# Kernel tuning notes

Measured on AMD Instinct MI355X. Metric: run time of the kernel, lower is better.

The kernel has to match this reference:

```python
import jax, jax.numpy as jnp
import numpy as np

B, T, IN, H, OUT, L = 1024, 128, 32, 256, 32, 3  # batch, times, input_dim, hidden_dim, output_dim, num_layers
STEP = 0.05  # odeint rk4 step_size; times grid is aligned to it


def lipswish(x):
    return 0.909 * x * jax.nn.sigmoid(x)


def setup_inputs() -> dict:
    key = jax.random.key(0)
    ks = jax.random.split(key, 4)
    coeffs = jax.random.normal(ks[0], (B, T, IN), dtype=jnp.float32)
    times = jnp.arange(T, dtype=jnp.float32) * STEP
    # learned parameters
    W_init = jax.random.normal(ks[1], (IN, H), dtype=jnp.float32) * (1.0 / np.sqrt(IN))
    b_init = jnp.zeros((H,), dtype=jnp.float32)
    # vector field f: L lipswish hidden layers + final linear, all H->H
    Wf = jax.random.normal(ks[2], (L + 1, H, H), dtype=jnp.float32) * (1.0 / np.sqrt(H))
    bf = jnp.zeros((L + 1, H), dtype=jnp.float32)
    Wd = jax.random.normal(ks[3], (H, OUT), dtype=jnp.float32) * (1.0 / np.sqrt(H))
    bd = jnp.zeros((OUT,), dtype=jnp.float32)
    return dict(coeffs=coeffs, times=times, W_init=W_init, b_init=b_init,
                Wf=Wf, bf=bf, Wd=Wd, bd=bd)


def reference(coeffs, times, W_init, b_init, Wf, bf, Wd, bd):
    # vector field func.f(t, y): autonomous MLP (inject_noise=False, so g unused)
    def f(y):
        h = y
        for i in range(L):
            h = lipswish(h @ Wf[i] + bf[i])
        return h @ Wf[L] + bf[L]

    # y0 = initial(X.evaluate(times))[:, 0, :] -> only the first time point seeds the state
    y0 = coeffs[:, 0, :] @ W_init + b_init  # [B, H]

    dts = times[1:] - times[:-1]  # each interval = one RK4 step (grid aligned to step_size)

    def step(y, dt):
        k1 = f(y)
        k2 = f(y + 0.5 * dt * k1)
        k3 = f(y + 0.5 * dt * k2)
        k4 = f(y + dt * k3)
        y_next = y + (dt / 6.0) * (k1 + 2.0 * k2 + 2.0 * k3 + k4)
        return y_next, y_next

    _, ys = jax.lax.scan(step, y0, dts)  # [T-1, B, H]
    z = jnp.concatenate([y0[None], ys], axis=0)  # [T, B, H]
    z = jnp.transpose(z, (1, 0, 2))  # [B, T, H]
    return z @ Wd + bd  # [B, T, OUT]
```

## Files before the change

### kernel.cpp

```cpp
#include <hip/hip_runtime.h>


#define T_ 128
#define IN_ 32
#define H_ 256

typedef _Float16 half8 __attribute__((ext_vector_type(8)));
typedef _Float16 half4 __attribute__((ext_vector_type(4)));
typedef float f32x4 __attribute__((ext_vector_type(4)));

__device__ __forceinline__ f32x4 mfma16(half8 a, half8 b, f32x4 c) {
    return __builtin_amdgcn_mfma_f32_16x16x32_f16(a, b, c, 0, 0, 0);
}

__device__ __forceinline__ half4 cvt4(f32x4 v) {
    half4 h;
    h[0] = (_Float16)v[0]; h[1] = (_Float16)v[1];
    h[2] = (_Float16)v[2]; h[3] = (_Float16)v[3];
    return h;
}

__device__ __forceinline__ f32x4 lips4(f32x4 v) {
    f32x4 r;
#pragma unroll
    for (int e = 0; e < 4; ++e) {
        float x = v[e];
        r[e] = 0.909f * x * __builtin_amdgcn_rcpf(1.f + __expf(-x));
    }
    return r;
}

#define RDH(KS, BUF) (*(const half8*)(ht + (BUF) + (((KS) & 1) ? (po + ((KS)-1)*64) : (pe + (KS)*64))))
#define RDA(C, KS)   (*(const half8*)(w0b + (C)*8192 + (KS)*1024))

#define KSTEP(LYI, KS, BREG) \
    acc0 = mfma16(wreg[LYI][0][KS], BREG, acc0); \
    acc1 = mfma16(wreg[LYI][1][KS], BREG, acc1);

#define LAYER_REG(LYI, BUF) do {                    \
    half8 b0 = RDH(0, BUF), b1 = RDH(1, BUF);       \
    KSTEP(LYI, 0, b0) b0 = RDH(2, BUF);             \
    KSTEP(LYI, 1, b1) b1 = RDH(3, BUF);             \
    KSTEP(LYI, 2, b0) b0 = RDH(4, BUF);             \
    KSTEP(LYI, 3, b1) b1 = RDH(5, BUF);             \
    KSTEP(LYI, 4, b0) b0 = RDH(6, BUF);             \
    KSTEP(LYI, 5, b1) b1 = RDH(7, BUF);             \
    KSTEP(LYI, 6, b0)                               \
    KSTEP(LYI, 7, b1)                               \
} while (0)

#define KSTEP0(KS, BREG) {                              \
    half8 x;                                            \
    x = RDA(0, KS); acc0 = mfma16(x, BREG, acc0);       \
    x = RDA(1, KS); acc1 = mfma16(x, BREG, acc1); }

#define LAYER_L0(BUF) do {                          \
    half8 b0 = RDH(0, BUF), b1 = RDH(1, BUF);       \
    KSTEP0(0, b0) b0 = RDH(2, BUF);                 \
    KSTEP0(1, b1) b1 = RDH(3, BUF);                 \
    KSTEP0(2, b0) b0 = RDH(4, BUF);                 \
    KSTEP0(3, b1) b1 = RDH(5, BUF);                 \
    KSTEP0(4, b0) b0 = RDH(6, BUF);                 \
    KSTEP0(5, b1) b1 = RDH(7, BUF);                 \
    KSTEP0(6, b0)                                   \
    KSTEP0(7, b1)                                   \
} while (0)

#define ACC_INIT(LY) do {                                       \
    acc0 = *(const f32x4*)(biasb + (LY)*1024 + 0);              \
    acc1 = *(const f32x4*)(biasb + (LY)*1024 + 64);             \
} while (0)

#define ACT_STORE(BUF) do {                                     \
    half4 s0 = cvt4(lips4(acc0)), s1 = cvt4(lips4(acc1));       \
    if (lr < 4) {                                               \
        *(half4*)(ht + (BUF) + wo0) = s0;                       \
        *(half4*)(ht + (BUF) + wo1) = s1;                       \
    }                                                           \
    __syncthreads();                                            \
} while (0)

#define STORE_Y(BUF, V0, V1) do {                               \
    half4 s0 = cvt4(V0), s1 = cvt4(V1);                         \
    if (lr < 4) {                                               \
        *(half4*)(ht + (BUF) + wo0) = s0;                       \
        *(half4*)(ht + (BUF) + wo1) = s1;                       \
    }                                                           \
} while (0)

__global__ __attribute__((amdgpu_flat_work_group_size(512, 512), amdgpu_waves_per_eu(2, 2)))
void ncde_kernel(const float* __restrict__ coeffs,
                 const float* __restrict__ times,
                 const float* __restrict__ W_init,
                 const float* __restrict__ b_init,
                 const float* __restrict__ Wf,
                 const float* __restrict__ bfv,
                 _Float16* __restrict__ ybuf)
{
    extern __shared__ char smem[];
    _Float16* w0   = (_Float16*)smem;
    char*     ht   = smem + 131072;
    float*    bias = (float*)(smem + 131072 + 4096);

    const int tid = threadIdx.x;
    const int l   = tid & 63;
    const int w   = tid >> 6;
    const int lr  = l & 15;
    const int lk  = l >> 4;
    const int rr  = l & 3;
    const int bc  = blockIdx.x;

    const int SWr = (rr << 4) ^ ((rr & 2) << 5);
    const int rb  = rr*512 + ((lk*16) ^ (SWr & 0x30));
    const int pe  = rb + (SWr & 0x40);
    const int po  = rb + (64 ^ (SWr & 0x40));
    const int SWw = ((lr & 3) << 4) ^ (((lr & 3) & 2) << 5);
    const int wo0 = (lr & 3)*512 + (((w*64) | (lk*8)) ^ SWw);
    const int wo1 = wo0 ^ 32;
    const char* w0b   = (const char*)w0 + (size_t)(2*w) * 8192 + l * 16;
    const char* biasb = (const char*)bias + w * 128 + lk * 16;

    for (int i = tid; i < 4 * H_; i += 512) bias[i] = bfv[i];

    for (int e = tid; e < 8192; e += 512) {
        int ct = e >> 9, ks = (e >> 6) & 7, ln = e & 63;
        const float* src = Wf + (size_t)(ks*32 + ((ln >> 4) << 3)) * H_ + ct*16 + (ln & 15);
        half8 v;
#pragma unroll
        for (int j = 0; j < 8; ++j) v[j] = (_Float16)src[(size_t)j * H_];
        *(half8*)(w0 + (size_t)e * 8) = v;
    }

    half8 wreg[3][2][8];
#pragma unroll
    for (int ly = 0; ly < 3; ++ly)
#pragma unroll
        for (int c = 0; c < 2; ++c)
#pragma unroll
            for (int ks = 0; ks < 8; ++ks) {
                const float* src = Wf + ((size_t)(ly + 1) * H_ + ks*32 + lk*8) * H_
                                      + w*32 + c*16 + lr;
                half8 v;
#pragma unroll
                for (int j = 0; j < 8; ++j) v[j] = (_Float16)src[(size_t)j * H_];
                wreg[ly][c][ks] = v;
            }

    f32x4 y0v, y1v;
    {
        const float* crow = coeffs + (size_t)(bc*4 + rr) * (T_ * IN_);
#pragma unroll
        for (int c = 0; c < 2; ++c) {
            f32x4 acc;
#pragma unroll
            for (int r = 0; r < 4; ++r) {
                int col = w*32 + c*16 + lk*4 + r;
                float s = b_init[col];
                for (int k = 0; k < IN_; ++k)
                    s += crow[k] * W_init[(size_t)k * H_ + col];
                acc[r] = s;
            }
            if (c == 0) y0v = acc; else y1v = acc;
        }
    }

    STORE_Y(0, y0v, y1v);
    __syncthreads();
    {
        if (tid < 128) {
            int drow = tid >> 5, dcb = (tid & 31) * 16;
            int dsw = (drow << 4) ^ ((drow & 2) << 5);
            uint4 v = *(const uint4*)(ht + drow*512 + (dcb ^ dsw));
            char* dst = (char*)ybuf + ((size_t)((bc >> 2) * T_)) * 8192
                        + (bc & 3) * 2048 + tid * 16;
            *(uint4*)dst = v;
        }
    }

#pragma unroll 1
    for (int st = 0; st < T_ - 1; ++st) {
        float dt = times[st + 1] - times[st];
        f32x4 ks0, ks1;
#pragma unroll 1
        for (int s = 0; s < 4; ++s) {
            f32x4 acc0, acc1;
            ACC_INIT(0); LAYER_L0(0);        ACT_STORE(2048);
            ACC_INIT(1); LAYER_REG(0, 2048); ACT_STORE(0);
            ACC_INIT(2); LAYER_REG(1, 0);    ACT_STORE(2048);
            ACC_INIT(3); LAYER_REG(2, 2048);
            if (s == 0)      { ks0 = acc0;       ks1 = acc1; }
            else if (s < 3)  { ks0 += 2.f*acc0;  ks1 += 2.f*acc1; }
            else             { ks0 += acc0;      ks1 += acc1; }
            if (s < 3) {
                float cy = (s == 2) ? dt : 0.5f * dt;
                STORE_Y(0, y0v + cy*acc0, y1v + cy*acc1);
            } else {
                float c6 = dt * (1.f / 6.f);
                y0v += c6*ks0; y1v += c6*ks1;
                STORE_Y(0, y0v, y1v);
            }
            __syncthreads();
        }
        {
            if (tid < 128) {
                int drow = tid >> 5, dcb = (tid & 31) * 16;
                int dsw = (drow << 4) ^ ((drow & 2) << 5);
                uint4 v = *(const uint4*)(ht + drow*512 + (dcb ^ dsw));
                char* dst = (char*)ybuf + ((size_t)((bc >> 2) * T_ + st + 1)) * 8192
                            + (bc & 3) * 2048 + tid * 16;
                *(uint4*)dst = v;
            }
        }
    }
}

__global__ __launch_bounds__(64)
void proj_kernel(const _Float16* __restrict__ ybuf,
                 const float* __restrict__ Wd,
                 const float* __restrict__ bd,
                 float* __restrict__ out)
{
    const int l  = threadIdx.x;
    const int lr = l & 15, lk = l >> 4;
    const int bc = blockIdx.x;
    const int tg = blockIdx.y;

    half8 wd[2][8];
#pragma unroll
    for (int c = 0; c < 2; ++c)
#pragma unroll
        for (int ks = 0; ks < 8; ++ks) {
            const float* src = Wd + (size_t)(ks*32 + lk*8) * 32 + c*16 + lr;
            half8 v;
#pragma unroll
            for (int j = 0; j < 8; ++j) v[j] = (_Float16)src[(size_t)j * 32];
            wd[c][ks] = v;
        }
    f32x4 bd0 = *(const f32x4*)(bd + lk*4);
    f32x4 bd1 = *(const f32x4*)(bd + 16 + lk*4);

    for (int t = tg*16; t < tg*16 + 16; ++t) {
        const _Float16* yt = ybuf + ((size_t)(bc*T_) + t) * 4096;
        f32x4 a0 = f32x4{0.f,0.f,0.f,0.f}, a1 = f32x4{0.f,0.f,0.f,0.f};
#pragma unroll
        for (int ks = 0; ks < 8; ++ks) {
            half8 b = *(const half8*)(yt + lr*256 + ks*32 + lk*8);
            a0 = mfma16(wd[0][ks], b, a0);
            a1 = mfma16(wd[1][ks], b, a1);
        }
        float* op = out + ((size_t)(bc*16 + lr) * T_ + t) * 32;
        *(f32x4*)(op + lk*4)      = a0 + bd0;
        *(f32x4*)(op + 16 + lk*4) = a1 + bd1;
    }
}

extern "C" void kernel_launch(void* const* d_in, const int* in_sizes, int n_in,
                              void* d_out, int out_size, void* d_ws, size_t ws_size,
                              hipStream_t stream) {
    const float* coeffs = (const float*)d_in[0];
    const float* times  = (const float*)d_in[1];
    const float* W_init = (const float*)d_in[2];
    const float* b_init = (const float*)d_in[3];
    const float* Wf     = (const float*)d_in[4];
    const float* bfv    = (const float*)d_in[5];
    const float* Wd     = (const float*)d_in[6];
    const float* bd     = (const float*)d_in[7];
    _Float16* ybuf = (_Float16*)d_ws;
    float* out = (float*)d_out;

    const size_t lds_bytes = 131072 + 4096 + 4096;
    hipLaunchKernelGGL(ncde_kernel, dim3(256), dim3(512), lds_bytes, stream,
                       coeffs, times, W_init, b_init, Wf, bfv, ybuf);
    hipLaunchKernelGGL(proj_kernel, dim3(64, 8), dim3(64), 0, stream,
                       ybuf, Wd, bd, out);
}
```

Baseline: 1.668 ms.

## Split hidden columns across 16 waves instead of 8 per block

Doubles the workgroup to 1024 threads so each wave owns one 16-column tile instead of two. Register-resident weights and accumulators are halved per wave, which allows 4 waves per EU instead of 2. The aim is more latency hiding on the serial MLP chain, since each wave's chain of dependent MFMAs gets shorter. In exchange, each barrier now synchronises twice as many waves, and every wave has to read the full shared activation operands from LDS, doubling LDS read traffic.

```diff
diff --git a/kernel.cpp b/kernel.cpp
--- a/kernel.cpp
+++ b/kernel.cpp
@@ -31,64 +31,46 @@
 }
 
 #define RDH(KS, BUF) (*(const half8*)(ht + (BUF) + (((KS) & 1) ? (po + ((KS)-1)*64) : (pe + (KS)*64))))
-#define RDA(C, KS)   (*(const half8*)(w0b + (C)*8192 + (KS)*1024))
-
-#define KSTEP(LYI, KS, BREG) \
-    acc0 = mfma16(wreg[LYI][0][KS], BREG, acc0); \
-    acc1 = mfma16(wreg[LYI][1][KS], BREG, acc1);
-
-#define LAYER_REG(LYI, BUF) do {                    \
-    half8 b0 = RDH(0, BUF), b1 = RDH(1, BUF);       \
-    KSTEP(LYI, 0, b0) b0 = RDH(2, BUF);             \
-    KSTEP(LYI, 1, b1) b1 = RDH(3, BUF);             \
-    KSTEP(LYI, 2, b0) b0 = RDH(4, BUF);             \
-    KSTEP(LYI, 3, b1) b1 = RDH(5, BUF);             \
-    KSTEP(LYI, 4, b0) b0 = RDH(6, BUF);             \
-    KSTEP(LYI, 5, b1) b1 = RDH(7, BUF);             \
-    KSTEP(LYI, 6, b0)                               \
-    KSTEP(LYI, 7, b1)                               \
-} while (0)
-
-#define KSTEP0(KS, BREG) {                              \
-    half8 x;                                            \
-    x = RDA(0, KS); acc0 = mfma16(x, BREG, acc0);       \
-    x = RDA(1, KS); acc1 = mfma16(x, BREG, acc1); }
-
-#define LAYER_L0(BUF) do {                          \
-    half8 b0 = RDH(0, BUF), b1 = RDH(1, BUF);       \
-    KSTEP0(0, b0) b0 = RDH(2, BUF);                 \
-    KSTEP0(1, b1) b1 = RDH(3, BUF);                 \
-    KSTEP0(2, b0) b0 = RDH(4, BUF);                 \
-    KSTEP0(3, b1) b1 = RDH(5, BUF);                 \
-    KSTEP0(4, b0) b0 = RDH(6, BUF);                 \
-    KSTEP0(5, b1) b1 = RDH(7, BUF);                 \
-    KSTEP0(6, b0)                                   \
-    KSTEP0(7, b1)                                   \
-} while (0)
-
-#define ACC_INIT(LY) do {                                       \
-    acc0 = *(const f32x4*)(biasb + (LY)*1024 + 0);              \
-    acc1 = *(const f32x4*)(biasb + (LY)*1024 + 64);             \
-} while (0)
-
-#define ACT_STORE(BUF) do {                                     \
-    half4 s0 = cvt4(lips4(acc0)), s1 = cvt4(lips4(acc1));       \
-    if (lr < 4) {                                               \
-        *(half4*)(ht + (BUF) + wo0) = s0;                       \
-        *(half4*)(ht + (BUF) + wo1) = s1;                       \
-    }                                                           \
-    __syncthreads();                                            \
-} while (0)
-
-#define STORE_Y(BUF, V0, V1) do {                               \
-    half4 s0 = cvt4(V0), s1 = cvt4(V1);                         \
-    if (lr < 4) {                                               \
-        *(half4*)(ht + (BUF) + wo0) = s0;                       \
-        *(half4*)(ht + (BUF) + wo1) = s1;                       \
-    }                                                           \
-} while (0)
-
-__global__ __attribute__((amdgpu_flat_work_group_size(512, 512), amdgpu_waves_per_eu(2, 2)))
+#define RDA(KS)      (*(const half8*)(w0b + (KS)*1024))
+
+#define LAYER_REG(LYI, BUF) do {                            \
+    half8 b0 = RDH(0, BUF), b1 = RDH(1, BUF);               \
+    acc0 = mfma16(wreg[LYI][0], b0, acc0); b0 = RDH(2, BUF);\
+    acc0 = mfma16(wreg[LYI][1], b1, acc0); b1 = RDH(3, BUF);\
+    acc0 = mfma16(wreg[LYI][2], b0, acc0); b0 = RDH(4, BUF);\
+    acc0 = mfma16(wreg[LYI][3], b1, acc0); b1 = RDH(5, BUF);\
+    acc0 = mfma16(wreg[LYI][4], b0, acc0); b0 = RDH(6, BUF);\
+    acc0 = mfma16(wreg[LYI][5], b1, acc0); b1 = RDH(7, BUF);\
+    acc0 = mfma16(wreg[LYI][6], b0, acc0);                  \
+    acc0 = mfma16(wreg[LYI][7], b1, acc0);                  \
+} while (0)
+
+#define LAYER_L0(BUF) do {                                  \
+    half8 b0 = RDH(0, BUF), b1 = RDH(1, BUF);               \
+    acc0 = mfma16(RDA(0), b0, acc0); b0 = RDH(2, BUF);      \
+    acc0 = mfma16(RDA(1), b1, acc0); b1 = RDH(3, BUF);      \
+    acc0 = mfma16(RDA(2), b0, acc0); b0 = RDH(4, BUF);      \
+    acc0 = mfma16(RDA(3), b1, acc0); b1 = RDH(5, BUF);      \
+    acc0 = mfma16(RDA(4), b0, acc0); b0 = RDH(6, BUF);      \
+    acc0 = mfma16(RDA(5), b1, acc0); b1 = RDH(7, BUF);      \
+    acc0 = mfma16(RDA(6), b0, acc0);                        \
+    acc0 = mfma16(RDA(7), b1, acc0);                        \
+} while (0)
+
+#define ACC_INIT(LY) do { acc0 = *(const f32x4*)(bias + (LY)*H_ + boff); } while (0)
+
+#define ACT_STORE(BUF) do {                                 \
+    half4 s0 = cvt4(lips4(acc0));                           \
+    if (lr < 4) *(half4*)(ht + (BUF) + wo0) = s0;           \
+    __syncthreads();                                        \
+} while (0)
+
+#define STORE_Y(BUF, V0) do {                               \
+    half4 s0 = cvt4(V0);                                    \
+    if (lr < 4) *(half4*)(ht + (BUF) + wo0) = s0;           \
+} while (0)
+
+__global__ __attribute__((amdgpu_flat_work_group_size(1024, 1024), amdgpu_waves_per_eu(4, 4)))
 void ncde_kernel(const float* __restrict__ coeffs,
                  const float* __restrict__ times,
                  const float* __restrict__ W_init,
@@ -115,14 +97,13 @@
     const int pe  = rb + (SWr & 0x40);
     const int po  = rb + (64 ^ (SWr & 0x40));
     const int SWw = ((lr & 3) << 4) ^ (((lr & 3) & 2) << 5);
-    const int wo0 = (lr & 3)*512 + (((w*64) | (lk*8)) ^ SWw);
-    const int wo1 = wo0 ^ 32;
-    const char* w0b   = (const char*)w0 + (size_t)(2*w) * 8192 + l * 16;
-    const char* biasb = (const char*)bias + w * 128 + lk * 16;
-
-    for (int i = tid; i < 4 * H_; i += 512) bias[i] = bfv[i];
-
-    for (int e = tid; e < 8192; e += 512) {
+    const int wo0 = (lr & 3)*512 + (((w*32) | (lk*8)) ^ SWw);
+    const int boff = w*16 + lk*4;
+    const char* w0b = (const char*)w0 + (size_t)w * 8192 + l * 16;
+
+    if (tid < 4 * H_) bias[tid] = bfv[tid];
+
+    for (int e = tid; e < 8192; e += 1024) {
         int ct = e >> 9, ks = (e >> 6) & 7, ln = e & 63;
         const float* src = Wf + (size_t)(ks*32 + ((ln >> 4) << 3)) * H_ + ct*16 + (ln & 15);
         half8 v;
@@ -131,40 +112,35 @@
         *(half8*)(w0 + (size_t)e * 8) = v;
     }
 
-    half8 wreg[3][2][8];
+    half8 wreg[3][8];
 #pragma unroll
     for (int ly = 0; ly < 3; ++ly)
 #pragma unroll
-        for (int c = 0; c < 2; ++c)
-#pragma unroll
-            for (int ks = 0; ks < 8; ++ks) {
-                const float* src = Wf + ((size_t)(ly + 1) * H_ + ks*32 + lk*8) * H_
-                                      + w*32 + c*16 + lr;
-                half8 v;
-#pragma unroll
-                for (int j = 0; j < 8; ++j) v[j] = (_Float16)src[(size_t)j * H_];
-                wreg[ly][c][ks] = v;
-            }
-
-    f32x4 y0v, y1v;
+        for (int ks = 0; ks < 8; ++ks) {
+            const float* src = Wf + ((size_t)(ly + 1) * H_ + ks*32 + lk*8) * H_
+                                  + w*16 + lr;
+            half8 v;
+#pragma unroll
+            for (int j = 0; j < 8; ++j) v[j] = (_Float16)src[(size_t)j * H_];
+            wreg[ly][ks] = v;
+        }
+
+    f32x4 y0v;
     {
         const float* crow = coeffs + (size_t)(bc*4 + rr) * (T_ * IN_);
-#pragma unroll
-        for (int c = 0; c < 2; ++c) {
-            f32x4 acc;
-#pragma unroll
-            for (int r = 0; r < 4; ++r) {
-                int col = w*32 + c*16 + lk*4 + r;
-                float s = b_init[col];
-                for (int k = 0; k < IN_; ++k)
-                    s += crow[k] * W_init[(size_t)k * H_ + col];
-                acc[r] = s;
-            }
-            if (c == 0) y0v = acc; else y1v = acc;
-        }
-    }
-
-    STORE_Y(0, y0v, y1v);
+        f32x4 acc;
+#pragma unroll
+        for (int r = 0; r < 4; ++r) {
+            int col = w*16 + lk*4 + r;
+            float s = b_init[col];
+            for (int k = 0; k < IN_; ++k)
+                s += crow[k] * W_init[(size_t)k * H_ + col];
+            acc[r] = s;
+        }
+        y0v = acc;
+    }
+
+    STORE_Y(0, y0v);
     __syncthreads();
     {
         if (tid < 128) {
@@ -180,24 +156,24 @@
 #pragma unroll 1
     for (int st = 0; st < T_ - 1; ++st) {
         float dt = times[st + 1] - times[st];
-        f32x4 ks0, ks1;
+        f32x4 ks0;
 #pragma unroll 1
         for (int s = 0; s < 4; ++s) {
-            f32x4 acc0, acc1;
+            f32x4 acc0;
             ACC_INIT(0); LAYER_L0(0);        ACT_STORE(2048);
             ACC_INIT(1); LAYER_REG(0, 2048); ACT_STORE(0);
             ACC_INIT(2); LAYER_REG(1, 0);    ACT_STORE(2048);
             ACC_INIT(3); LAYER_REG(2, 2048);
-            if (s == 0)      { ks0 = acc0;       ks1 = acc1; }
-            else if (s < 3)  { ks0 += 2.f*acc0;  ks1 += 2.f*acc1; }
-            else             { ks0 += acc0;      ks1 += acc1; }
+            if (s == 0)      ks0 = acc0;
+            else if (s < 3)  ks0 += 2.f*acc0;
+            else             ks0 += acc0;
             if (s < 3) {
                 float cy = (s == 2) ? dt : 0.5f * dt;
-                STORE_Y(0, y0v + cy*acc0, y1v + cy*acc1);
+                STORE_Y(0, y0v + cy*acc0);
             } else {
                 float c6 = dt * (1.f / 6.f);
-                y0v += c6*ks0; y1v += c6*ks1;
-                STORE_Y(0, y0v, y1v);
+                y0v += c6*ks0;
+                STORE_Y(0, y0v);
             }
             __syncthreads();
         }
@@ -269,7 +245,7 @@
     float* out = (float*)d_out;
 
     const size_t lds_bytes = 131072 + 4096 + 4096;
-    hipLaunchKernelGGL(ncde_kernel, dim3(256), dim3(512), lds_bytes, stream,
+    hipLaunchKernelGGL(ncde_kernel, dim3(256), dim3(1024), lds_bytes, stream,
                        coeffs, times, W_init, b_init, Wf, bfv, ybuf);
     hipLaunchKernelGGL(proj_kernel, dim3(64, 8), dim3(64), 0, stream,
                        ybuf, Wd, bd, out);
```

After: 2.874 ms. 72.3% more time.
